# Performance work log

Measured on AMD Instinct MI355X. Metric: run time of the kernel, lower is better.

The kernel has to match this reference:

```python
import jax, jax.numpy as jnp
import numpy as np
from jax import lax

THR = 1.0            # spike_threshold
GRAD_WIDTH = 0.5     # sinabs SingleExponential grad_width
GRAD_SCALE = 1.0     # sinabs SingleExponential grad_scale
ABS_WIDTH = THR * GRAD_WIDTH

# SingleSpike with SingleExponential surrogate gradient (Shrestha & Orchard 2018)
@jax.custom_vjp
def spike(v):
    return (v >= THR).astype(v.dtype)

def _spike_fwd(v):
    return (v >= THR).astype(v.dtype), v

def _spike_bwd(v, g):
    sg = (GRAD_SCALE / ABS_WIDTH) * jnp.exp(-jnp.abs(v - THR) / ABS_WIDTH)
    return (g * sg,)

spike.defvjp(_spike_fwd, _spike_bwd)

def avgpool4(x):  # AvgPool2d(4) on NCHW
    n, c, h, w = x.shape
    return x.reshape(n, c, h // 4, 4, w // 4, 4).mean(axis=(3, 5))

def conv7(x, w):  # Conv2d k=7 pad=3 no bias, NCHW/OIHW
    return lax.conv_general_dilated(x, w, (1, 1), [(3, 3), (3, 3)],
                                    dimension_numbers=('NCHW', 'OIHW', 'NCHW'))

def iaf(x):
    """IAF with MembraneSubtract reset. x: (n, t, c, h, w) -> spikes, same shape."""
    xt = jnp.moveaxis(x, 1, 0)  # (t, n, c, h, w)
    def step(v, xin):
        v = v + xin
        s = spike(v)
        return v - s * THR, s
    _, s = lax.scan(step, jnp.zeros_like(xt[0]), xt)
    return jnp.moveaxis(s, 0, 1)

def setup_inputs() -> dict:
    key = jax.random.key(0)
    k0, k1, k2, k3 = jax.random.split(key, 4)
    inp = jax.random.uniform(k0, (8, 2, 256, 256, 64), dtype=jnp.float32)
    w0 = jax.random.normal(k1, (4, 2, 7, 7), jnp.float32) / np.float32(np.sqrt(2 * 49))
    w1 = jax.random.normal(k2, (8, 4, 7, 7), jnp.float32) / np.float32(np.sqrt(4 * 49))
    wl = jax.random.normal(k3, (2, 128), jnp.float32) / np.float32(np.sqrt(128))
    return {"inp": inp, "w0": w0, "w1": w1, "wl": wl}

def reference(inp, w0, w1, wl):
    n, c, y, x, t = inp.shape
    # movedim(-1, 1) then flatten(0, 1): (n, t, c, y, x) -> (n*t, c, y, x)
    data = jnp.moveaxis(inp, -1, 1).reshape(n * t, c, y, x)
    h0 = conv7(avgpool4(data), w0)                          # (n*t, 4, 64, 64)
    s0 = iaf(h0.reshape(n, t, 4, 64, 64)).reshape(n * t, 4, 64, 64)
    h1 = conv7(avgpool4(s0), w1)                            # (n*t, 8, 16, 16)
    s1 = iaf(h1.reshape(n, t, 8, 16, 16)).reshape(n * t, 8, 16, 16)
    feat = avgpool4(s1).reshape(n * t, -1)                  # (n*t, 128)
    out = feat @ wl.T                                       # (n*t, 2)
    return jnp.moveaxis(out.reshape(n, t, 2), 1, -1)        # (n, 2, t)
```

## Files before the change

kernel.cpp:

```cpp
#include <hip/hip_runtime.h>


#define OFF_P0   0
#define OFF_P1   12582912
#define OFF_H1   13107200
#define OFF_FT   14155776

typedef float f32x4 __attribute__((ext_vector_type(4)));

__global__ __launch_bounds__(256) void pool0_kernel(
        const float* __restrict__ inp, float* __restrict__ out) {
    int tid = blockIdx.x * blockDim.x + threadIdx.x;
    int t4 = tid & 15;
    int px = (tid >> 4) & 63;
    int py = (tid >> 10) & 63;
    int nc = tid >> 16;
    const float* base = inp + (size_t)nc * 4194304 + (size_t)t4 * 4;
    int y0 = py * 4, x0 = px * 4;
    float a0 = 0.f, a1 = 0.f, a2 = 0.f, a3 = 0.f;
    #pragma unroll
    for (int dy = 0; dy < 4; ++dy) {
        const float* row = base + ((size_t)(y0 + dy) * 256 + x0) * 64;
        #pragma unroll
        for (int dx = 0; dx < 4; ++dx) {
            const f32x4 v = __builtin_nontemporal_load(
                (const f32x4*)(row + dx * 64));
            a0 += v.x; a1 += v.y; a2 += v.z; a3 += v.w;
        }
    }
    float4 o = make_float4(a0 * 0.0625f, a1 * 0.0625f,
                           a2 * 0.0625f, a3 * 0.0625f);
    ((float4*)out)[tid] = o;
}

__global__ __launch_bounds__(512) void conv0_iaf0_pool1_kernel(
        const float* __restrict__ pooled0, const float* __restrict__ w0,
        float* __restrict__ pooled1) {
    __shared__ float w[392];
    __shared__ float tile[8192];

    for (int i = threadIdx.x; i < 392; i += blockDim.x) w[i] = w0[i];

    int b   = blockIdx.x;
    int pxb = b & 7;
    int pyo = (b >> 3) & 15;
    int n   = b >> 7;

    int tid = threadIdx.x;
    int t4  = tid & 15;
    int pxl = (tid >> 4) & 7;
    int pr  = tid >> 7;
    int px  = pxb * 8 + pxl;
    int py  = pyo * 4 + pr;

    __syncthreads();

    float acc[4][4] = {};
    bool interior = (pyo >= 1) & (pyo <= 14) & (pxb >= 1) & (pxb <= 6);
    if (interior) {
        for (int ic = 0; ic < 2; ++ic) {
            const float* in_c = pooled0 + (size_t)(n * 2 + ic) * 262144
                              + (size_t)t4 * 4 + (size_t)(px - 3) * 64;
            const float* wic = w + ic * 49;
            #pragma unroll
            for (int ky = 0; ky < 7; ++ky) {
                const float* in_row = in_c + (size_t)(py - 3 + ky) * 4096;
                #pragma unroll
                for (int kx = 0; kx < 7; ++kx) {
                    float4 v = *(const float4*)(in_row + kx * 64);
                    #pragma unroll
                    for (int oc = 0; oc < 4; ++oc) {
                        float wd = wic[oc * 98 + ky * 7 + kx];
                        acc[oc][0] += v.x * wd;
                        acc[oc][1] += v.y * wd;
                        acc[oc][2] += v.z * wd;
                        acc[oc][3] += v.w * wd;
                    }
                }
            }
        }
    } else {
        for (int ic = 0; ic < 2; ++ic) {
            const float* in_c = pooled0 + (size_t)(n * 2 + ic) * 262144
                              + (size_t)t4 * 4;
            const float* wic = w + ic * 49;
            #pragma unroll
            for (int ky = 0; ky < 7; ++ky) {
                int iy = py - 3 + ky;
                if (iy < 0 || iy >= 64) continue;
                const float* in_row = in_c + (size_t)iy * 4096;
                #pragma unroll
                for (int kx = 0; kx < 7; ++kx) {
                    int ix = px + kx - 3;
                    if (ix < 0 || ix >= 64) continue;
                    float4 v = *(const float4*)(in_row + ix * 64);
                    #pragma unroll
                    for (int oc = 0; oc < 4; ++oc) {
                        float wd = wic[oc * 98 + ky * 7 + kx];
                        acc[oc][0] += v.x * wd;
                        acc[oc][1] += v.y * wd;
                        acc[oc][2] += v.z * wd;
                        acc[oc][3] += v.w * wd;
                    }
                }
            }
        }
    }
    #pragma unroll
    for (int oc = 0; oc < 4; ++oc) {
        int p = oc * 32 + pr * 8 + pxl;
        #pragma unroll
        for (int j = 0; j < 4; ++j) {
            int tt = t4 * 4 + j;
            tile[p * 64 + ((tt + p) & 63)] = acc[oc][j];
        }
    }
    __syncthreads();

    if (tid < 128) {
        int p   = tid;
        int oc  = p >> 5;
        int pxo = (p >> 2) & 1;
        float v = 0.f;
        unsigned int sp[16];
        const float* tp = tile + p * 64;
        #pragma unroll
        for (int i = 0; i < 16; ++i) {
            unsigned int wd = 0;
            #pragma unroll
            for (int j = 0; j < 4; ++j) {
                int t = i * 4 + j;
                float x = tp[(t + p) & 63];
                v += x;
                unsigned int s_ = (v >= 1.f) ? 1u : 0u;
                v -= (float)s_;
                wd += s_ << (8 * j);
            }
            sp[i] = wd;
        }
        #pragma unroll
        for (int i = 0; i < 16; ++i) {
            sp[i] += __shfl_xor(sp[i], 1);
            sp[i] += __shfl_xor(sp[i], 2);
            sp[i] += __shfl_xor(sp[i], 8);
            sp[i] += __shfl_xor(sp[i], 16);
        }
        int i = (p & 3) | (((p >> 3) & 3) << 2);
        unsigned int s = sp[i];
        float4 o = make_float4((float)(s & 255u)         * 0.0625f,
                               (float)((s >> 8)  & 255u) * 0.0625f,
                               (float)((s >> 16) & 255u) * 0.0625f,
                               (float)((s >> 24) & 255u) * 0.0625f);
        float* outp = pooled1 +
            (((size_t)(n * 4 + oc) * 16 + pyo) * 16 + (pxb * 2 + pxo)) * 64 + i * 4;
        *(float4*)outp = o;
    }
}

__global__ __launch_bounds__(256) void conv1_kernel(
        const float* __restrict__ pooled1,
        const float* __restrict__ w1,
        float* __restrict__ h1) {
    __shared__ float w[1568];
    for (int i = threadIdx.x; i < 1568; i += blockDim.x) w[i] = w1[i];
    __syncthreads();

    int tid = blockIdx.x * blockDim.x + threadIdx.x;
    int t4 = tid & 15;
    int px = (tid >> 4) & 15;
    int py = (tid >> 8) & 15;
    int og = (tid >> 12) & 1;
    int n  = tid >> 13;

    float acc[4][4] = {};

    for (int ic = 0; ic < 4; ++ic) {
        const float* in_c = pooled1 + (size_t)(n * 4 + ic) * 16384 + t4 * 4;
        const float* wic = w + (size_t)og * 4 * 196 + ic * 49;
        #pragma unroll
        for (int ky = 0; ky < 7; ++ky) {
            int iy = py + ky - 3;
            if (iy < 0 || iy >= 16) continue;
            const float* in_row = in_c + (size_t)iy * 1024;
            #pragma unroll
            for (int kx = 0; kx < 7; ++kx) {
                int ix = px + kx - 3;
                if (ix < 0 || ix >= 16) continue;
                float4 v = *(const float4*)(in_row + ix * 64);
                #pragma unroll
                for (int oc4 = 0; oc4 < 4; ++oc4) {
                    float wd = wic[oc4 * 196 + ky * 7 + kx];
                    acc[oc4][0] += v.x * wd;
                    acc[oc4][1] += v.y * wd;
                    acc[oc4][2] += v.z * wd;
                    acc[oc4][3] += v.w * wd;
                }
            }
        }
    }
    size_t ob = (size_t)n * 131072 + (size_t)(og * 4) * 16384
              + (size_t)py * 1024 + px * 64 + t4 * 4;
    #pragma unroll
    for (int oc4 = 0; oc4 < 4; ++oc4) {
        float4 o = make_float4(acc[oc4][0], acc[oc4][1],
                               acc[oc4][2], acc[oc4][3]);
        *(float4*)(h1 + ob + (size_t)oc4 * 16384) = o;
    }
}

__global__ __launch_bounds__(256) void iaf1_pool2_kernel(
        const float* __restrict__ h1, float* __restrict__ feat) {
    int b = blockIdx.x;
    int c = b & 7;
    int n = b >> 3;
    int tid = threadIdx.x;
    int dx  = tid & 3;
    int dy  = (tid >> 2) & 3;
    int q   = tid >> 4;
    int pyo = q >> 2;
    int pxo = q & 3;
    int py  = pyo * 4 + dy;
    int px  = pxo * 4 + dx;

    const float4* p = (const float4*)(h1 +
        (((size_t)(n * 8 + c) * 16 + py) * 16 + px) * 64);

    float v = 0.f;
    unsigned int sp[16];
    #pragma unroll
    for (int i = 0; i < 16; ++i) {
        float4 x = p[i];
        unsigned int w = 0;
        #define STEP(j, e)                                                    \
        {   v += x.e;                                                         \
            unsigned int s_ = (v >= 1.f) ? 1u : 0u;                           \
            v -= (float)s_;                                                   \
            w += s_ << (8 * j); }
        STEP(0, x) STEP(1, y) STEP(2, z) STEP(3, w)
        #undef STEP
        sp[i] = w;
    }
    #pragma unroll
    for (int i = 0; i < 16; ++i) {
        sp[i] += __shfl_xor(sp[i], 1);
        sp[i] += __shfl_xor(sp[i], 2);
        sp[i] += __shfl_xor(sp[i], 4);
        sp[i] += __shfl_xor(sp[i], 8);
    }
    int i = tid & 15;
    unsigned int s = sp[i];
    float4 o = make_float4((float)(s & 255u)         * 0.0625f,
                           (float)((s >> 8)  & 255u) * 0.0625f,
                           (float)((s >> 16) & 255u) * 0.0625f,
                           (float)((s >> 24) & 255u) * 0.0625f);
    int f = c * 16 + q;
    *(float4*)(feat + ((size_t)n * 128 + f) * 64 + i * 4) = o;
}

__global__ __launch_bounds__(64) void linear_kernel(
        const float* __restrict__ feat, const float* __restrict__ wl,
        float* __restrict__ out) {
    int tid = blockIdx.x * 64 + threadIdx.x;
    int t = tid & 63;
    int j = (tid >> 6) & 1;
    int n = tid >> 7;
    const float* fp = feat + (size_t)n * 128 * 64 + t;
    const float* wp = wl + j * 128;
    double acc = 0.0;
    for (int f = 0; f < 128; ++f)
        acc += (double)wp[f] * (double)fp[(size_t)f * 64];
    out[(size_t)(n * 2 + j) * 64 + t] = (float)acc;
}

extern "C" void kernel_launch(void* const* d_in, const int* in_sizes, int n_in,
                              void* d_out, int out_size, void* d_ws, size_t ws_size,
                              hipStream_t stream) {
    const float* inp = (const float*)d_in[0];
    const float* w0  = (const float*)d_in[1];
    const float* w1  = (const float*)d_in[2];
    const float* wl  = (const float*)d_in[3];
    float* out = (float*)d_out;
    float* ws  = (float*)d_ws;

    float* pooled0 = ws + OFF_P0;
    float* pooled1 = ws + OFF_P1;
    float* h1      = ws + OFF_H1;
    float* feat    = ws + OFF_FT;

    pool0_kernel<<<4096, 256, 0, stream>>>(inp, pooled0);
    conv0_iaf0_pool1_kernel<<<1024, 512, 0, stream>>>(pooled0, w0, pooled1);
    conv1_kernel<<<256, 256, 0, stream>>>(pooled1, w1, h1);
    iaf1_pool2_kernel<<<64, 256, 0, stream>>>(h1, feat);
    linear_kernel<<<16, 64, 0, stream>>>(feat, wl, out);
}
```

Baseline: 454.0 us.

## Stage conv0 input halo tile in shared memory with zero padding

The conv0 kernel now cooperatively loads a zero-padded 10x14 halo tile of pooled0 for each input channel into LDS, then runs the 7x7 convolution from shared memory instead of issuing 49 global float4 loads per thread. This removes the separate interior and boundary code paths and cuts the redundant global/L2 traffic between neighbouring threads. The row stride is padded to 68 floats to limit bank conflicts. The cost is extra barriers, a larger LDS footprint (about 38KB) aliased with the output tile, and possibly lower occupancy.

```diff
diff --git a/kernel.cpp b/kernel.cpp
--- a/kernel.cpp
+++ b/kernel.cpp
@@ -37,7 +37,9 @@
         const float* __restrict__ pooled0, const float* __restrict__ w0,
         float* __restrict__ pooled1) {
     __shared__ float w[392];
-    __shared__ float tile[8192];
+    __shared__ float smem[9520];
+    float* ins  = smem;
+    float* tile = smem;
 
     for (int i = threadIdx.x; i < 392; i += blockDim.x) w[i] = w0[i];
 
@@ -50,62 +52,45 @@
     int t4  = tid & 15;
     int pxl = (tid >> 4) & 7;
     int pr  = tid >> 7;
-    int px  = pxb * 8 + pxl;
-    int py  = pyo * 4 + pr;
-
-    __syncthreads();
+    int py0 = pyo * 4;
 
     float acc[4][4] = {};
-    bool interior = (pyo >= 1) & (pyo <= 14) & (pxb >= 1) & (pxb <= 6);
-    if (interior) {
-        for (int ic = 0; ic < 2; ++ic) {
-            const float* in_c = pooled0 + (size_t)(n * 2 + ic) * 262144
-                              + (size_t)t4 * 4 + (size_t)(px - 3) * 64;
-            const float* wic = w + ic * 49;
+
+    for (int ic = 0; ic < 2; ++ic) {
+        __syncthreads();
+        const float* src = pooled0 + (size_t)(n * 2 + ic) * 262144;
+        for (int c = tid; c < 2240; c += 512) {
+            int row = c / 224;
+            int rem = c - row * 224;
+            int px  = rem >> 4;
+            int tt  = rem & 15;
+            int iy  = py0 - 3 + row;
+            int ix  = pxb * 8 - 3 + px;
+            f32x4 v = {0.f, 0.f, 0.f, 0.f};
+            if (iy >= 0 && iy < 64 && ix >= 0 && ix < 64)
+                v = *(const f32x4*)(src + (size_t)iy * 4096 + ix * 64 + tt * 4);
+            *(f32x4*)(ins + row * 952 + px * 68 + tt * 4) = v;
+        }
+        __syncthreads();
+        const float* wic = w + ic * 49;
+        #pragma unroll
+        for (int ky = 0; ky < 7; ++ky) {
+            const float* rbase = ins + (pr + ky) * 952 + pxl * 68 + t4 * 4;
             #pragma unroll
-            for (int ky = 0; ky < 7; ++ky) {
-                const float* in_row = in_c + (size_t)(py - 3 + ky) * 4096;
+            for (int kx = 0; kx < 7; ++kx) {
+                f32x4 v = *(const f32x4*)(rbase + kx * 68);
                 #pragma unroll
-                for (int kx = 0; kx < 7; ++kx) {
-                    float4 v = *(const float4*)(in_row + kx * 64);
-                    #pragma unroll
-                    for (int oc = 0; oc < 4; ++oc) {
-                        float wd = wic[oc * 98 + ky * 7 + kx];
-                        acc[oc][0] += v.x * wd;
-                        acc[oc][1] += v.y * wd;
-                        acc[oc][2] += v.z * wd;
-                        acc[oc][3] += v.w * wd;
-                    }
+                for (int oc = 0; oc < 4; ++oc) {
+                    float wd = wic[oc * 98 + ky * 7 + kx];
+                    acc[oc][0] += v.x * wd;
+                    acc[oc][1] += v.y * wd;
+                    acc[oc][2] += v.z * wd;
+                    acc[oc][3] += v.w * wd;
                 }
             }
         }
-    } else {
-        for (int ic = 0; ic < 2; ++ic) {
-            const float* in_c = pooled0 + (size_t)(n * 2 + ic) * 262144
-                              + (size_t)t4 * 4;
-            const float* wic = w + ic * 49;
-            #pragma unroll
-            for (int ky = 0; ky < 7; ++ky) {
-                int iy = py - 3 + ky;
-                if (iy < 0 || iy >= 64) continue;
-                const float* in_row = in_c + (size_t)iy * 4096;
-                #pragma unroll
-                for (int kx = 0; kx < 7; ++kx) {
-                    int ix = px + kx - 3;
-                    if (ix < 0 || ix >= 64) continue;
-                    float4 v = *(const float4*)(in_row + ix * 64);
-                    #pragma unroll
-                    for (int oc = 0; oc < 4; ++oc) {
-                        float wd = wic[oc * 98 + ky * 7 + kx];
-                        acc[oc][0] += v.x * wd;
-                        acc[oc][1] += v.y * wd;
-                        acc[oc][2] += v.z * wd;
-                        acc[oc][3] += v.w * wd;
-                    }
-                }
-            }
-        }
-    }
+    }
+    __syncthreads();
     #pragma unroll
     for (int oc = 0; oc < 4; ++oc) {
         int p = oc * 32 + pr * 8 + pxl;
```

After: 440.0 us. 1.03x faster.
